# Kernel tuning notes

Hardware: AMD Instinct MI355X
Metric: run time of the kernel (lower is better)

## Reference

```python
import jax, jax.numpy as jnp
import numpy as np

N = 100000      # nodes
E = 1600000     # edges (avg degree 16)
IN = 64         # in_feats
OUT = 64        # out_feats per head
H = 4           # heads
SLOPE = 0.2     # leaky relu negative slope


def setup_inputs() -> dict:
    key = jax.random.key(0)
    ks = jax.random.split(key, 6)
    feat = jax.random.normal(ks[0], (N, IN), dtype=jnp.float32)
    # xavier-ish scale for weights
    W_weight = jax.random.normal(ks[1], (OUT * H, IN), dtype=jnp.float32) * (2.0 / (IN + OUT * H)) ** 0.5
    W_bias = jnp.zeros((OUT * H,), dtype=jnp.float32)
    a_l = jax.random.normal(ks[2], (1, OUT, H), dtype=jnp.float32) * 0.1
    a_r = jax.random.normal(ks[3], (1, OUT, H), dtype=jnp.float32) * 0.1
    row = jax.random.randint(ks[4], (E,), 0, N, dtype=jnp.int32)
    col = jax.random.randint(ks[5], (E,), 0, N, dtype=jnp.int32)
    return {"feat": feat, "W_weight": W_weight, "W_bias": W_bias,
            "a_l": a_l, "a_r": a_r, "row": row, "col": col}


def reference(feat, W_weight, W_bias, a_l, a_r, row, col):
    n = feat.shape[0]
    # linear projection -> [N, OUT, H]
    Z = (feat @ W_weight.T + W_bias).reshape(n, OUT, H)
    # per-node attention logits [N, H]
    e_l = (Z * a_l).sum(axis=1)
    e_r = (Z * a_r).sum(axis=1)
    # edge scores + leaky relu [E, H]
    e = e_l[row] + e_r[col]
    a = jnp.where(e > 0, e, SLOPE * e)
    # segment softmax over incoming edges of each destination row
    m = jax.ops.segment_max(a, row, num_segments=n)          # [N, H]
    ex = jnp.exp(a - m[row])                                  # [E, H]
    s = jax.ops.segment_sum(ex, row, num_segments=n)          # [N, H]
    alpha = ex / s[row]                                       # [E, H]
    # weighted aggregation: out[i,:,h] = sum_{e: row[e]=i} alpha[e,h] * Z[col[e],:,h]
    msg = alpha[:, None, :] * Z[col]                          # [E, OUT, H]
    out = jax.ops.segment_sum(msg, row, num_segments=n)       # [N, OUT, H]
    return out.reshape(n, -1)
```

## Files before the change

### kernel.cpp

```cpp
#include <hip/hip_runtime.h>
#include <stdint.h>

#define SLOPE  0.2f
#define PN     64
#define CAP    64

typedef float    f32x4 __attribute__((ext_vector_type(4)));
typedef _Float16 h16x2 __attribute__((ext_vector_type(2)));

union FU { float f; unsigned int u; };
union HU { unsigned int u; h16x2 h; };
__device__ __forceinline__ float ubits(unsigned int u) { FU c; c.u = u; return c.f; }

__global__ __launch_bounds__(256) void prep_kernel(
    const float* __restrict__ W, const float* __restrict__ bias,
    const float* __restrict__ a_l, const float* __restrict__ a_r,
    unsigned int* __restrict__ WtHu, float* __restrict__ biasP,
    float* __restrict__ Wl, float* __restrict__ bl)
{
    int t = threadIdx.x;
    if (blockIdx.x < 32) {
        int g = blockIdx.x * 256 + t;
        int kk = g >> 8, cp = g & 255;
        int o = (cp & 63) * 4 + (cp >> 6);
        HU u;
        u.h = (h16x2){ (_Float16)W[o * 64 + 2 * kk], (_Float16)W[o * 64 + 2 * kk + 1] };
        WtHu[kk * 256 + cp] = u.u;
    } else {
        for (int id = t; id < 512; id += 256) {
            int x = id >> 6, k = id & 63;
            int h = x & 3;
            const float* v = (x < 4) ? a_l : a_r;
            float s = 0.f;
            for (int d = 0; d < 64; d++) {
                int o = d * 4 + h;
                s += v[o] * W[o * 64 + k];
            }
            Wl[id] = s;
        }
        if (t < 8) {
            int h = t & 3;
            const float* v = (t < 4) ? a_l : a_r;
            float s = 0.f;
            for (int d = 0; d < 64; d++) { int o = d * 4 + h; s += v[o] * bias[o]; }
            bl[t] = s;
        }
        {
            int cp = t;
            int o = (cp & 63) * 4 + (cp >> 6);
            biasP[cp] = bias[o];
        }
    }
}

__global__ __launch_bounds__(256) void proj_kernel(
    const float4* __restrict__ feat4,
    const float* __restrict__ Wl, const float* __restrict__ bl,
    uint2* __restrict__ featb2,
    float* __restrict__ el, float* __restrict__ er, int N)
{
    __shared__ float fT[64][68];
    __shared__ float WlS[8][68];
    __shared__ float blS[8];

    int t = threadIdx.x;
    int nodeBase = blockIdx.x * PN;

    for (int p = t; p < PN * 16; p += 256) {
        int n = p >> 4, kq = p & 15;
        int gn = nodeBase + n;
        float4 v = make_float4(0.f, 0.f, 0.f, 0.f);
        if (gn < N) v = feat4[(size_t)gn * 16 + kq];
        fT[kq * 4 + 0][n] = v.x; fT[kq * 4 + 1][n] = v.y;
        fT[kq * 4 + 2][n] = v.z; fT[kq * 4 + 3][n] = v.w;
        if (gn < N) {
            HU u0, u1;
            u0.h = (h16x2){ (_Float16)v.x, (_Float16)v.y };
            u1.h = (h16x2){ (_Float16)v.z, (_Float16)v.w };
            featb2[(size_t)gn * 16 + kq] = make_uint2(u0.u, u1.u);
        }
    }
    for (int p = t; p < 512; p += 256) WlS[p >> 6][p & 63] = Wl[p];
    if (t < 8) blS[t] = bl[t];
    __syncthreads();

    for (int r = 0; r < 2; r++) {
        int id = t + 256 * r;
        int n = id >> 3, x = id & 7;
        int gn = nodeBase + n;
        if (gn < N) {
            float e = blS[x];
            #pragma unroll 8
            for (int k = 0; k < 64; k++) e += fT[k][n] * WlS[x][k];
            if (x < 4) el[(size_t)gn * 4 + x] = e;
            else       er[(size_t)gn * 4 + (x - 4)] = e;
        }
    }
}

__global__ __launch_bounds__(256) void scatter_kernel(
    const int* __restrict__ row, const int* __restrict__ col,
    int* __restrict__ cnt, int* __restrict__ csr, int E)
{
    int e = blockIdx.x * 256 + threadIdx.x;
    if (e < E) {
        int r = row[e];
        int pos = atomicAdd(&cnt[r], 1);
        if (pos < CAP) csr[(size_t)r * CAP + pos] = col[e];
    }
}

__global__ __launch_bounds__(256) void gat_aggregate(
    const uint2* __restrict__ featb2,
    const float* __restrict__ el, const float* __restrict__ er,
    const int* __restrict__ cnt, const int* __restrict__ csr,
    uint2* __restrict__ agg, int N)
{
    __shared__ float aL[4][64];
    __shared__ int   cL[4][16];

    int t = threadIdx.x, lane = t & 63, w = t >> 6;
    int i = blockIdx.x * 4 + w;
    if (i >= N) return;

    int start = i * CAP;
    int dg = min(cnt[i], CAP);
    int eL = lane >> 2, hh = lane & 3;
    int hsel = lane >> 4, kq = lane & 15;
    float elh = el[(size_t)i * 4 + hh];

    float m = -3.0e38f;
    float m_h = -3.0e38f;
    float l = 0.f;
    float a0 = 0.f, a1 = 0.f, a2 = 0.f, a3 = 0.f;

    int c = 0;
    if (eL < dg) c = csr[start + eL];

    for (int base = 0; base < dg; base += 16) {
        int cnt2 = min(16, dg - base);
        bool full = (cnt2 > 8);

        if (hh == 0) cL[w][eL] = c;

        float ev = er[(size_t)c * 4 + hh];

        uint2 fq[16];
        #pragma unroll
        for (int j = 0; j < 2; j++) {
            int4 c4 = *(const int4*)&cL[w][4 * j];
            fq[4 * j + 0] = featb2[(size_t)c4.x * 16 + kq];
            fq[4 * j + 1] = featb2[(size_t)c4.y * 16 + kq];
            fq[4 * j + 2] = featb2[(size_t)c4.z * 16 + kq];
            fq[4 * j + 3] = featb2[(size_t)c4.w * 16 + kq];
        }
        if (full) {
            #pragma unroll
            for (int j = 2; j < 4; j++) {
                int4 c4 = *(const int4*)&cL[w][4 * j];
                fq[4 * j + 0] = featb2[(size_t)c4.x * 16 + kq];
                fq[4 * j + 1] = featb2[(size_t)c4.y * 16 + kq];
                fq[4 * j + 2] = featb2[(size_t)c4.z * 16 + kq];
                fq[4 * j + 3] = featb2[(size_t)c4.w * 16 + kq];
            }
        }

        int rem = dg - base - 16;
        int cn = 0;
        if (rem > 0 && eL < rem) cn = csr[start + base + 16 + eL];

        float e  = elh + ev;
        float sc = (eL < cnt2) ? (e > 0.f ? e : SLOPE * e) : -3.0e38f;
        float v = sc;
        v = fmaxf(v, __shfl_xor(v, 4));
        v = fmaxf(v, __shfl_xor(v, 8));
        v = fmaxf(v, __shfl_xor(v, 16));
        v = fmaxf(v, __shfl_xor(v, 32));
        float mnew = fmaxf(m, v);
        float a = __expf(sc - mnew);
        float sv = a;
        sv += __shfl_xor(sv, 4);
        sv += __shfl_xor(sv, 8);
        sv += __shfl_xor(sv, 16);
        sv += __shfl_xor(sv, 32);
        l = l * __expf(m - mnew) + sv;
        m = mnew;

        aL[w][hh * 16 + eL] = a;

        float mn_h = __shfl(mnew, hsel);
        float r = __expf(m_h - mn_h);
        a0 *= r; a1 *= r; a2 *= r; a3 *= r;
        m_h = mn_h;

        #pragma unroll
        for (int j = 0; j < 2; j++) {
            f32x4 al4 = *(const f32x4*)&aL[w][hsel * 16 + 4 * j];
            #pragma unroll
            for (int q = 0; q < 4; q++) {
                float al = al4[q];
                HU hx, hy; hx.u = fq[4 * j + q].x; hy.u = fq[4 * j + q].y;
                a0 += al * (float)hx.h[0];
                a1 += al * (float)hx.h[1];
                a2 += al * (float)hy.h[0];
                a3 += al * (float)hy.h[1];
            }
        }
        if (full) {
            #pragma unroll
            for (int j = 2; j < 4; j++) {
                f32x4 al4 = *(const f32x4*)&aL[w][hsel * 16 + 4 * j];
                #pragma unroll
                for (int q = 0; q < 4; q++) {
                    float al = al4[q];
                    HU hx, hy; hx.u = fq[4 * j + q].x; hy.u = fq[4 * j + q].y;
                    a0 += al * (float)hx.h[0];
                    a1 += al * (float)hx.h[1];
                    a2 += al * (float)hy.h[0];
                    a3 += al * (float)hy.h[1];
                }
            }
        }
        c = cn;
    }

    float lh  = __shfl(l, hsel);
    float inv = (lh > 0.f) ? 1.0f / lh : 0.f;
    HU p0, p1;
    p0.h = (h16x2){ (_Float16)(a0 * inv), (_Float16)(a1 * inv) };
    p1.h = (h16x2){ (_Float16)(a2 * inv), (_Float16)(a3 * inv) };
    agg[(size_t)i * 64 + lane] = make_uint2(p0.u, p1.u);
}

__global__ __launch_bounds__(256) void gemm_kernel(
    const uint4* __restrict__ agg4,
    const uint4* __restrict__ WtH4,
    const float* __restrict__ biasP,
    const int* __restrict__ cnt,
    float* __restrict__ out, int N)
{
    __shared__ char smem[32768 + 17408 + 128];
    unsigned int* WtS   = (unsigned int*)smem;
    unsigned int* aggSu = (unsigned int*)(smem + 32768);
    int*          cntS  = (int*)(smem + 32768 + 17408);
    float*        obS   = (float*)smem;

    int t = threadIdx.x;
    int nodeBase = blockIdx.x * 32;

    #pragma unroll
    for (int p = 0; p < 8; p++)
        *(uint4*)&WtS[(p * 256 + t) * 4] = WtH4[p * 256 + t];
    for (int p = t; p < 1024; p += 256) {
        int n = p >> 5, q = p & 31;
        int gn = nodeBase + n;
        uint4 v = make_uint4(0u, 0u, 0u, 0u);
        if (gn < N) v = agg4[(size_t)gn * 32 + q];
        *(uint4*)&aggSu[n * 132 + q * 4] = v;
    }
    if (t < 32) { int gn = nodeBase + t; cntS[t] = (gn < N) ? cnt[gn] : 0; }
    __syncthreads();

    int cg = t & 31, ng = t >> 5;
    int h = cg >> 3;
    float acc[4][8];
    #pragma unroll
    for (int u = 0; u < 4; u++)
        #pragma unroll
        for (int j = 0; j < 8; j++) acc[u][j] = 0.f;

    for (int kk = 0; kk < 32; kk++) {
        uint4 wv0 = *(const uint4*)&WtS[kk * 256 + cg * 8];
        uint4 wv1 = *(const uint4*)&WtS[kk * 256 + cg * 8 + 4];
        unsigned int au[4];
        #pragma unroll
        for (int u = 0; u < 4; u++)
            au[u] = aggSu[(ng * 4 + u) * 132 + h * 32 + kk];
        HU wp[8];
        wp[0].u = wv0.x; wp[1].u = wv0.y; wp[2].u = wv0.z; wp[3].u = wv0.w;
        wp[4].u = wv1.x; wp[5].u = wv1.y; wp[6].u = wv1.z; wp[7].u = wv1.w;
        #pragma unroll
        for (int u = 0; u < 4; u++) {
            HU av; av.u = au[u];
            #pragma unroll
            for (int j = 0; j < 8; j++)
                acc[u][j] = __builtin_amdgcn_fdot2(av.h, wp[j].h, acc[u][j], false);
        }
    }

    float4 b0 = *(const float4*)&biasP[cg * 8];
    float4 b1 = *(const float4*)&biasP[cg * 8 + 4];
    float bj[8] = { b0.x, b0.y, b0.z, b0.w, b1.x, b1.y, b1.z, b1.w };
    int bq[4];
    #pragma unroll
    for (int u = 0; u < 4; u++) bq[u] = cntS[ng * 4 + u];
    __syncthreads();

    #pragma unroll
    for (int u = 0; u < 4; u++) {
        int n = ng * 4 + u;
        float bsc = (bq[u] > 0) ? 1.f : 0.f;
        f32x4 x0 = { acc[u][0] + bsc * bj[0], acc[u][1] + bsc * bj[1],
                     acc[u][2] + bsc * bj[2], acc[u][3] + bsc * bj[3] };
        f32x4 x1 = { acc[u][4] + bsc * bj[4], acc[u][5] + bsc * bj[5],
                     acc[u][6] + bsc * bj[6], acc[u][7] + bsc * bj[7] };
        *(f32x4*)&obS[n * 264 + cg * 8]     = x0;
        *(f32x4*)&obS[n * 264 + cg * 8 + 4] = x1;
    }
    __syncthreads();

    int ln = t >> 3, part = t & 7;
    int gn = nodeBase + ln;
    if (gn < N) {
        #pragma unroll
        for (int k = 0; k < 8; k++) {
            int d = k * 8 + part;
            f32x4 o4 = { obS[ln * 264 +   0 + d], obS[ln * 264 +  64 + d],
                         obS[ln * 264 + 128 + d], obS[ln * 264 + 192 + d] };
            __builtin_nontemporal_store(o4, (f32x4*)(out + (size_t)gn * 256) + d);
        }
    }
}

extern "C" void kernel_launch(void* const* d_in, const int* in_sizes, int n_in,
                              void* d_out, int out_size, void* d_ws, size_t ws_size,
                              hipStream_t stream)
{
    const float* feat  = (const float*)d_in[0];
    const float* W     = (const float*)d_in[1];
    const float* bias  = (const float*)d_in[2];
    const float* a_l   = (const float*)d_in[3];
    const float* a_r   = (const float*)d_in[4];
    const int*   row   = (const int*)d_in[5];
    const int*   col   = (const int*)d_in[6];
    float* out = (float*)d_out;

    int N = in_sizes[0] / 64;
    int E = in_sizes[5];

    char* ws = (char*)d_ws;
    size_t off = 0;
    auto alloc = [&](size_t bytes) -> void* {
        void* p = (void*)(ws + off);
        off += (bytes + 255) & ~(size_t)255;
        return p;
    };
    unsigned short* featb = (unsigned short*)alloc((size_t)N * 64 * sizeof(unsigned short));
    unsigned int*   WtHu  = (unsigned int*)alloc(8192 * sizeof(unsigned int));
    float*          biasP = (float*)alloc(256 * sizeof(float));
    float* el    = (float*)alloc((size_t)N * 4 * sizeof(float));
    float* er    = (float*)alloc((size_t)N * 4 * sizeof(float));
    float* Wl    = (float*)alloc(512 * sizeof(float));
    float* bl    = (float*)alloc(8 * sizeof(float));
    int*   cnt   = (int*)alloc((size_t)N * sizeof(int));
    int*   csr   = (int*)alloc((size_t)N * CAP * sizeof(int));
    uint2* agg   = (uint2*)alloc((size_t)N * 64 * sizeof(uint2));
    (void)ws_size; (void)n_in; (void)out_size;

    hipMemsetAsync(cnt, 0, (size_t)N * sizeof(int), stream);
    prep_kernel<<<33, 256, 0, stream>>>(W, bias, a_l, a_r, WtHu, biasP, Wl, bl);
    proj_kernel<<<(N + PN - 1) / PN, 256, 0, stream>>>(
        (const float4*)feat, Wl, bl, (uint2*)featb, el, er, N);
    scatter_kernel<<<(E + 255) / 256, 256, 0, stream>>>(row, col, cnt, csr, E);
    gat_aggregate<<<(N + 3) / 4, 256, 0, stream>>>(
        (const uint2*)featb, el, er, cnt, csr, agg, N);
    gemm_kernel<<<(N + 31) / 32, 256, 0, stream>>>(
        (const uint4*)agg, (const uint4*)WtHu, biasP, cnt, out, N);
}
```

Before: 352.0 us.

## Partition scatter and aggregate rows by XCD for L2 locality; fold count zeroing into prep

The scatter and aggregate kernels now map blocks so that each XCD (blockIdx mod 8) owns a contiguous eighth of the destination rows. In scatter, every edge is read by all 8 XCD groups but only the owning group does the atomic and CSR write, so those stay in one XCD's L2. The aggregate kernel uses the same row-to-XCD mapping so the CSR and count reads hit the L2 that wrote them. The memset of the counts is folded into the prep kernel as extra blocks. The cost is that scatter reads row[] 8 times over, and the scheme assumes round-robin block dispatch across XCDs.

```diff
diff --git a/kernel.cpp b/kernel.cpp
--- a/kernel.cpp
+++ b/kernel.cpp
@@ -4,6 +4,7 @@
 #define SLOPE  0.2f
 #define PN     64
 #define CAP    64
+#define NXCD   8
 
 typedef float    f32x4 __attribute__((ext_vector_type(4)));
 typedef _Float16 h16x2 __attribute__((ext_vector_type(2)));
@@ -16,7 +17,8 @@
     const float* __restrict__ W, const float* __restrict__ bias,
     const float* __restrict__ a_l, const float* __restrict__ a_r,
     unsigned int* __restrict__ WtHu, float* __restrict__ biasP,
-    float* __restrict__ Wl, float* __restrict__ bl)
+    float* __restrict__ Wl, float* __restrict__ bl,
+    int* __restrict__ cnt, int N)
 {
     int t = threadIdx.x;
     if (blockIdx.x < 32) {
@@ -26,7 +28,7 @@
         HU u;
         u.h = (h16x2){ (_Float16)W[o * 64 + 2 * kk], (_Float16)W[o * 64 + 2 * kk + 1] };
         WtHu[kk * 256 + cp] = u.u;
-    } else {
+    } else if (blockIdx.x == 32) {
         for (int id = t; id < 512; id += 256) {
             int x = id >> 6, k = id & 63;
             int h = x & 3;
@@ -50,6 +52,9 @@
             int o = (cp & 63) * 4 + (cp >> 6);
             biasP[cp] = bias[o];
         }
+    } else {
+        int i = (blockIdx.x - 33) * 256 + t;
+        if (i < N) cnt[i] = 0;
     }
 }
 
@@ -100,13 +105,23 @@
 
 __global__ __launch_bounds__(256) void scatter_kernel(
     const int* __restrict__ row, const int* __restrict__ col,
-    int* __restrict__ cnt, int* __restrict__ csr, int E)
-{
-    int e = blockIdx.x * 256 + threadIdx.x;
-    if (e < E) {
-        int r = row[e];
-        int pos = atomicAdd(&cnt[r], 1);
-        if (pos < CAP) csr[(size_t)r * CAP + pos] = col[e];
+    int* __restrict__ cnt, int* __restrict__ csr, int E, int rng, int N)
+{
+    int xcd = blockIdx.x & (NXCD - 1);
+    int chunk = blockIdx.x >> 3;
+    int rlo = xcd * rng;
+    int rhi = min(rlo + rng, N);
+    int base = chunk * 1024 + threadIdx.x;
+    #pragma unroll
+    for (int q = 0; q < 4; q++) {
+        int e = base + q * 256;
+        if (e < E) {
+            int r = row[e];
+            if (r >= rlo && r < rhi) {
+                int pos = atomicAdd(&cnt[r], 1);
+                if (pos < CAP) csr[(size_t)r * CAP + pos] = col[e];
+            }
+        }
     }
 }
 
@@ -114,14 +129,17 @@
     const uint2* __restrict__ featb2,
     const float* __restrict__ el, const float* __restrict__ er,
     const int* __restrict__ cnt, const int* __restrict__ csr,
-    uint2* __restrict__ agg, int N)
+    uint2* __restrict__ agg, int N, int rng)
 {
     __shared__ float aL[4][64];
     __shared__ int   cL[4][16];
 
     int t = threadIdx.x, lane = t & 63, w = t >> 6;
-    int i = blockIdx.x * 4 + w;
-    if (i >= N) return;
+    int xcd = blockIdx.x & (NXCD - 1);
+    int j = blockIdx.x >> 3;
+    int local = j * 4 + w;
+    int i = xcd * rng + local;
+    if (local >= rng || i >= N) return;
 
     int start = i * CAP;
     int dg = min(cnt[i], CAP);
@@ -147,21 +165,21 @@
 
         uint2 fq[16];
         #pragma unroll
-        for (int j = 0; j < 2; j++) {
-            int4 c4 = *(const int4*)&cL[w][4 * j];
-            fq[4 * j + 0] = featb2[(size_t)c4.x * 16 + kq];
-            fq[4 * j + 1] = featb2[(size_t)c4.y * 16 + kq];
-            fq[4 * j + 2] = featb2[(size_t)c4.z * 16 + kq];
-            fq[4 * j + 3] = featb2[(size_t)c4.w * 16 + kq];
+        for (int jj = 0; jj < 2; jj++) {
+            int4 c4 = *(const int4*)&cL[w][4 * jj];
+            fq[4 * jj + 0] = featb2[(size_t)c4.x * 16 + kq];
+            fq[4 * jj + 1] = featb2[(size_t)c4.y * 16 + kq];
+            fq[4 * jj + 2] = featb2[(size_t)c4.z * 16 + kq];
+            fq[4 * jj + 3] = featb2[(size_t)c4.w * 16 + kq];
         }
         if (full) {
             #pragma unroll
-            for (int j = 2; j < 4; j++) {
-                int4 c4 = *(const int4*)&cL[w][4 * j];
-                fq[4 * j + 0] = featb2[(size_t)c4.x * 16 + kq];
-                fq[4 * j + 1] = featb2[(size_t)c4.y * 16 + kq];
-                fq[4 * j + 2] = featb2[(size_t)c4.z * 16 + kq];
-                fq[4 * j + 3] = featb2[(size_t)c4.w * 16 + kq];
+            for (int jj = 2; jj < 4; jj++) {
+                int4 c4 = *(const int4*)&cL[w][4 * jj];
+                fq[4 * jj + 0] = featb2[(size_t)c4.x * 16 + kq];
+                fq[4 * jj + 1] = featb2[(size_t)c4.y * 16 + kq];
+                fq[4 * jj + 2] = featb2[(size_t)c4.z * 16 + kq];
+                fq[4 * jj + 3] = featb2[(size_t)c4.w * 16 + kq];
             }
         }
 
@@ -194,12 +212,12 @@
         m_h = mn_h;
 
         #pragma unroll
-        for (int j = 0; j < 2; j++) {
-            f32x4 al4 = *(const f32x4*)&aL[w][hsel * 16 + 4 * j];
+        for (int jj = 0; jj < 2; jj++) {
+            f32x4 al4 = *(const f32x4*)&aL[w][hsel * 16 + 4 * jj];
             #pragma unroll
             for (int q = 0; q < 4; q++) {
                 float al = al4[q];
-                HU hx, hy; hx.u = fq[4 * j + q].x; hy.u = fq[4 * j + q].y;
+                HU hx, hy; hx.u = fq[4 * jj + q].x; hy.u = fq[4 * jj + q].y;
                 a0 += al * (float)hx.h[0];
                 a1 += al * (float)hx.h[1];
                 a2 += al * (float)hy.h[0];
@@ -208,12 +226,12 @@
         }
         if (full) {
             #pragma unroll
-            for (int j = 2; j < 4; j++) {
-                f32x4 al4 = *(const f32x4*)&aL[w][hsel * 16 + 4 * j];
+            for (int jj = 2; jj < 4; jj++) {
+                f32x4 al4 = *(const f32x4*)&aL[w][hsel * 16 + 4 * jj];
                 #pragma unroll
                 for (int q = 0; q < 4; q++) {
                     float al = al4[q];
-                    HU hx, hy; hx.u = fq[4 * j + q].x; hy.u = fq[4 * j + q].y;
+                    HU hx, hy; hx.u = fq[4 * jj + q].x; hy.u = fq[4 * jj + q].y;
                     a0 += al * (float)hx.h[0];
                     a1 += al * (float)hx.h[1];
                     a2 += al * (float)hy.h[0];
@@ -357,13 +375,17 @@
     uint2* agg   = (uint2*)alloc((size_t)N * 64 * sizeof(uint2));
     (void)ws_size; (void)n_in; (void)out_size;
 
-    hipMemsetAsync(cnt, 0, (size_t)N * sizeof(int), stream);
-    prep_kernel<<<33, 256, 0, stream>>>(W, bias, a_l, a_r, WtHu, biasP, Wl, bl);
+    int rng = (N + NXCD - 1) / NXCD;
+    int ZB  = (N + 255) / 256;
+    int EC  = (E + 1023) / 1024;
+    int GB  = (rng + 3) / 4;
+
+    prep_kernel<<<33 + ZB, 256, 0, stream>>>(W, bias, a_l, a_r, WtHu, biasP, Wl, bl, cnt, N);
     proj_kernel<<<(N + PN - 1) / PN, 256, 0, stream>>>(
         (const float4*)feat, Wl, bl, (uint2*)featb, el, er, N);
-    scatter_kernel<<<(E + 255) / 256, 256, 0, stream>>>(row, col, cnt, csr, E);
-    gat_aggregate<<<(N + 3) / 4, 256, 0, stream>>>(
-        (const uint2*)featb, el, er, cnt, csr, agg, N);
+    scatter_kernel<<<EC * NXCD, 256, 0, stream>>>(row, col, cnt, csr, E, rng, N);
+    gat_aggregate<<<GB * NXCD, 256, 0, stream>>>(
+        (const uint2*)featb, el, er, cnt, csr, agg, N, rng);
     gemm_kernel<<<(N + 31) / 32, 256, 0, stream>>>(
         (const uint4*)agg, (const uint4*)WtHu, biasP, cnt, out, N);
 }
```

New measurement: 337.9 us. 1.04x faster.
